# Optimization experiments

Measured on AMD Instinct MI355X. Metric: run time of the kernel, lower is better.

Reference implementation:

```python
import jax, jax.numpy as jnp
import numpy as np

N, E, D, H, SEQ = 50000, 600000, 128, 128, 50


def _gcn(x, W, b, src, dst):
    # PyG GCNConv: D^{-1/2}(A+I)D^{-1/2} X W + b, edge weights = 1
    n = x.shape[0]
    h = x @ W  # [N, H]
    deg = jnp.zeros((n,), x.dtype).at[dst].add(1.0) + 1.0  # +1 for self loop
    dinv = jax.lax.rsqrt(deg)
    norm = dinv[src] * dinv[dst]  # [E]
    agg = jnp.zeros_like(h).at[dst].add(h[src] * norm[:, None])
    agg = agg + h * (dinv * dinv)[:, None]  # self-loop contribution
    return agg + b


def _lstm_layer(xs, w_ih, w_hh, b_ih, b_hh):
    # xs: [B, T, I]; PyTorch gate order i, f, g, o
    B = xs.shape[0]
    Hh = w_hh.shape[1]
    bias = b_ih + b_hh

    def step(carry, x_t):
        h, c = carry
        g = x_t @ w_ih.T + h @ w_hh.T + bias
        i, f, gg, o = jnp.split(g, 4, axis=-1)
        c = jax.nn.sigmoid(f) * c + jax.nn.sigmoid(i) * jnp.tanh(gg)
        h = jax.nn.sigmoid(o) * jnp.tanh(c)
        return (h, c), h

    init = (jnp.zeros((B, Hh), xs.dtype), jnp.zeros((B, Hh), xs.dtype))
    _, hs = jax.lax.scan(step, init, xs.transpose(1, 0, 2))
    return hs.transpose(1, 0, 2)  # [B, T, H]


def setup_inputs() -> dict:
    key = jax.random.key(0)
    ks = jax.random.split(key, 16)
    s = 1.0 / np.sqrt(H)
    inp = {
        "x": jax.random.normal(ks[0], (N, D), jnp.float32),
        "edge_index": jax.random.randint(ks[1], (2, E), 0, N, jnp.int64),
        "sequence_length": SEQ,
        "W1": jax.random.normal(ks[2], (D, H), jnp.float32) * s,
        "b1": jnp.zeros((H,), jnp.float32),
        "W2": jax.random.normal(ks[3], (H, H), jnp.float32) * s,
        "b2": jnp.zeros((H,), jnp.float32),
        "fc_w": jax.random.normal(ks[4], (1, H), jnp.float32) * s,
        "fc_b": jnp.zeros((1,), jnp.float32),
    }
    for l in range(2):
        inp[f"w_ih{l}"] = jax.random.normal(ks[5 + 4 * l], (4 * H, H), jnp.float32) * s
        inp[f"w_hh{l}"] = jax.random.normal(ks[6 + 4 * l], (4 * H, H), jnp.float32) * s
        inp[f"b_ih{l}"] = jax.random.normal(ks[7 + 4 * l], (4 * H,), jnp.float32) * s
        inp[f"b_hh{l}"] = jax.random.normal(ks[8 + 4 * l], (4 * H,), jnp.float32) * s
    return inp


def reference(x, edge_index, sequence_length, W1, b1, W2, b2,
              w_ih0, w_hh0, b_ih0, b_hh0, w_ih1, w_hh1, b_ih1, b_hh1,
              fc_w, fc_b):
    src, dst = edge_index[0], edge_index[1]
    h = jax.nn.relu(_gcn(x, W1, b1, src, dst))   # dropout is identity in eval
    h = jax.nn.relu(_gcn(h, W2, b2, src, dst))
    seq = h.reshape(-1, sequence_length, h.shape[-1])  # [B, T, H]
    seq = _lstm_layer(seq, w_ih0, w_hh0, b_ih0, b_hh0)
    seq = _lstm_layer(seq, w_ih1, w_hh1, b_ih1, b_hh1)
    last = seq[:, -1, :]
    return last @ fc_w.T + fc_b  # [B, 1]
```

## Files before the change

### kernel.cpp

```cpp
#include <hip/hip_runtime.h>

#define NND 50000
#define NE  600000
#define TSEQ 50
#define NB  1000
#define SB  4
#define AHS 136
#define NSCB 196

typedef __attribute__((ext_vector_type(4))) float f32x4;
typedef __attribute__((ext_vector_type(8))) short s16x8;

__device__ __forceinline__ float sigf(float x) {
    return __builtin_amdgcn_rcpf(1.0f + __expf(-x));
}
__device__ __forceinline__ float tanhfast(float x) {
    x = fminf(fmaxf(x, -15.f), 15.f);
    float e = __expf(2.f * x);
    return (e - 1.f) * __builtin_amdgcn_rcpf(e + 1.f);
}
__device__ __forceinline__ unsigned short f2bf(float f) {
    unsigned int u = __float_as_uint(f);
    u = u + 0x7FFFu + ((u >> 16) & 1u);
    return (unsigned short)(u >> 16);
}
__device__ __forceinline__ float bf2f(unsigned short h) {
    return __uint_as_float(((unsigned int)h) << 16);
}
__device__ __forceinline__ void barrier_lds_only() {
    asm volatile("s_waitcnt lgkmcnt(0)\n\ts_barrier" ::: "memory");
}
__device__ __forceinline__ int grow_perm(int n) {
    int grp = n / 200;
    int rem = n % 200;
    return grp * 200 + (n % 50) * 4 + rem / 50;
}

__global__ void k_count(const int* __restrict__ ei, int* __restrict__ cnt) {
    int e = blockIdx.x * 256 + threadIdx.x;
    if (e < NE) atomicAdd(&cnt[ei[NE + e]], 1);
}

__global__ __launch_bounds__(256) void k_bsum(const int* __restrict__ cnt,
                                              int* __restrict__ bsum) {
    __shared__ int red[256];
    int t = threadIdx.x;
    int idx = blockIdx.x * 256 + t;
    red[t] = (idx < NND) ? cnt[idx] : 0;
    __syncthreads();
    for (int off = 128; off > 0; off >>= 1) {
        if (t < off) red[t] += red[t + off];
        __syncthreads();
    }
    if (t == 0) bsum[blockIdx.x] = red[0];
}

__global__ __launch_bounds__(256) void k_bscan(int* __restrict__ bsum) {
    __shared__ int ps[256];
    int t = threadIdx.x;
    int v = (t < NSCB) ? bsum[t] : 0;
    ps[t] = v;
    __syncthreads();
    for (int off = 1; off < 256; off <<= 1) {
        int u = 0;
        if (t >= off) u = ps[t - off];
        __syncthreads();
        if (t >= off) ps[t] += u;
        __syncthreads();
    }
    if (t < NSCB) bsum[t] = ps[t] - v;
}

__global__ __launch_bounds__(256) void k_bout(const int* __restrict__ cnt,
                                              const int* __restrict__ bsum,
                                              int* __restrict__ rowstart,
                                              float* __restrict__ dinv) {
    __shared__ int ps[256];
    int t = threadIdx.x;
    int idx = blockIdx.x * 256 + t;
    int v = (idx < NND) ? cnt[idx] : 0;
    ps[t] = v;
    __syncthreads();
    for (int off = 1; off < 256; off <<= 1) {
        int u = 0;
        if (t >= off) u = ps[t - off];
        __syncthreads();
        if (t >= off) ps[t] += u;
        __syncthreads();
    }
    int boff = bsum[blockIdx.x];
    if (idx < NND) {
        rowstart[idx] = boff + ps[t] - v;
        dinv[idx] = 1.0f / sqrtf((float)v + 1.0f);
    }
    if (idx == NND - 1) rowstart[NND] = boff + ps[t];
}

__global__ void k_fill(const int* __restrict__ ei, const int* __restrict__ rowstart,
                       int* __restrict__ cursor, int* __restrict__ adj) {
    int e = blockIdx.x * 256 + threadIdx.x;
    if (e >= NE) return;
    int s = ei[e], d = ei[NE + e];
    int pos = atomicAdd(&cursor[d], 1);
    adj[rowstart[d] + pos] = s;
}

__global__ __launch_bounds__(256) void k_gemm_mfma_h2(
    const unsigned short* __restrict__ Ahi,
    const unsigned short* __restrict__ Bhi, const unsigned short* __restrict__ Blo,
    const float* __restrict__ bias, unsigned short* __restrict__ C,
    int M, int Nc, int NT)
{
    __shared__ unsigned short As_hi[128][136];

    const int tid  = threadIdx.x;
    const int lane = tid & 63, wave = tid >> 6;
    const int mw = wave & 1, nw = wave >> 1;
    const int l15 = lane & 15, quad = lane >> 4;
    const int rowBase = blockIdx.y * 128;

    {
        int r0 = tid >> 4;
        int ko = (tid & 15) * 8;
        #pragma unroll
        for (int i = 0; i < 8; ++i) {
            int row = r0 + i * 16;
            int g = rowBase + row;
            uint4 vh = make_uint4(0, 0, 0, 0);
            if (g < M) vh = *(const uint4*)&Ahi[(size_t)g * 128 + ko];
            *(uint4*)&As_hi[row][ko] = vh;
        }
    }
    __syncthreads();

    for (int nt = 0; nt < NT; ++nt) {
        const int colBase = (blockIdx.x * NT + nt) * 64;

        s16x8 bh[2][4], bl[2][4];
        #pragma unroll
        for (int ns = 0; ns < 2; ++ns) {
            int gn = colBase + nw * 32 + ns * 16 + l15;
            #pragma unroll
            for (int kq = 0; kq < 4; ++kq) {
                bh[ns][kq] = *(const s16x8*)&Bhi[(size_t)gn * 128 + kq * 32 + quad * 8];
                bl[ns][kq] = *(const s16x8*)&Blo[(size_t)gn * 128 + kq * 32 + quad * 8];
            }
        }

        f32x4 acc[4][2] = {};
        #pragma unroll
        for (int kq = 0; kq < 4; ++kq) {
            int kof = kq * 32 + quad * 8;
            s16x8 ah[4];
            #pragma unroll
            for (int ms = 0; ms < 4; ++ms) {
                int r = mw * 64 + ms * 16 + l15;
                ah[ms] = *(const s16x8*)&As_hi[r][kof];
            }
            #pragma unroll
            for (int ms = 0; ms < 4; ++ms)
                #pragma unroll
                for (int ns = 0; ns < 2; ++ns)
                    acc[ms][ns] = __builtin_amdgcn_mfma_f32_16x16x32_bf16(ah[ms], bh[ns][kq], acc[ms][ns], 0, 0, 0);
            #pragma unroll
            for (int ms = 0; ms < 4; ++ms)
                #pragma unroll
                for (int ns = 0; ns < 2; ++ns)
                    acc[ms][ns] = __builtin_amdgcn_mfma_f32_16x16x32_bf16(ah[ms], bl[ns][kq], acc[ms][ns], 0, 0, 0);
        }

        #pragma unroll
        for (int ns = 0; ns < 2; ++ns) {
            int col = colBase + nw * 32 + ns * 16 + l15;
            float bv = bias ? bias[col] : 0.f;
            #pragma unroll
            for (int ms = 0; ms < 4; ++ms) {
                int row0 = rowBase + mw * 64 + ms * 16 + quad * 4;
                #pragma unroll
                for (int r = 0; r < 4; ++r) {
                    int row = row0 + r;
                    if (row < M) C[(size_t)row * Nc + col] = f2bf(acc[ms][ns][r] + bv);
                }
            }
        }
    }
}

__global__ __launch_bounds__(256) void k_gemm_mfma_xa(
    const float* __restrict__ X,
    const unsigned short* __restrict__ Bhi, const unsigned short* __restrict__ Blo,
    const float* __restrict__ bias, unsigned short* __restrict__ C,
    int M, int Nc, int NT)
{
    __shared__ unsigned short As_hi[128][136];
    __shared__ unsigned short As_lo[128][136];

    const int tid  = threadIdx.x;
    const int lane = tid & 63, wave = tid >> 6;
    const int mw = wave & 1, nw = wave >> 1;
    const int l15 = lane & 15, quad = lane >> 4;
    const int rowBase = blockIdx.y * 128;

    {
        int r0 = tid >> 4;
        int ko = (tid & 15) * 8;
        #pragma unroll
        for (int i = 0; i < 8; ++i) {
            int row = r0 + i * 16;
            int g = rowBase + row;
            unsigned short hx[8], lx[8];
            if (g < M) {
                float4 v0 = *(const float4*)&X[(size_t)g * 128 + ko];
                float4 v1 = *(const float4*)&X[(size_t)g * 128 + ko + 4];
                const float vv[8] = {v0.x, v0.y, v0.z, v0.w, v1.x, v1.y, v1.z, v1.w};
                #pragma unroll
                for (int e = 0; e < 8; ++e) {
                    hx[e] = f2bf(vv[e]);
                    lx[e] = f2bf(vv[e] - bf2f(hx[e]));
                }
            } else {
                #pragma unroll
                for (int e = 0; e < 8; ++e) { hx[e] = 0; lx[e] = 0; }
            }
            *(uint4*)&As_hi[row][ko] = *(const uint4*)hx;
            *(uint4*)&As_lo[row][ko] = *(const uint4*)lx;
        }
    }
    __syncthreads();

    for (int nt = 0; nt < NT; ++nt) {
        const int colBase = (blockIdx.x * NT + nt) * 64;

        s16x8 bh[2][4], bl[2][4];
        #pragma unroll
        for (int ns = 0; ns < 2; ++ns) {
            int gn = colBase + nw * 32 + ns * 16 + l15;
            #pragma unroll
            for (int kq = 0; kq < 4; ++kq) {
                bh[ns][kq] = *(const s16x8*)&Bhi[(size_t)gn * 128 + kq * 32 + quad * 8];
                bl[ns][kq] = *(const s16x8*)&Blo[(size_t)gn * 128 + kq * 32 + quad * 8];
            }
        }

        f32x4 acc[4][2] = {};
        #pragma unroll
        for (int kq = 0; kq < 4; ++kq) {
            int kof = kq * 32 + quad * 8;
            s16x8 ah[4], al[4];
            #pragma unroll
            for (int ms = 0; ms < 4; ++ms) {
                int r = mw * 64 + ms * 16 + l15;
                ah[ms] = *(const s16x8*)&As_hi[r][kof];
                al[ms] = *(const s16x8*)&As_lo[r][kof];
            }
            #pragma unroll
            for (int ms = 0; ms < 4; ++ms)
                #pragma unroll
                for (int ns = 0; ns < 2; ++ns)
                    acc[ms][ns] = __builtin_amdgcn_mfma_f32_16x16x32_bf16(ah[ms], bh[ns][kq], acc[ms][ns], 0, 0, 0);
            #pragma unroll
            for (int ms = 0; ms < 4; ++ms)
                #pragma unroll
                for (int ns = 0; ns < 2; ++ns)
                    acc[ms][ns] = __builtin_amdgcn_mfma_f32_16x16x32_bf16(al[ms], bh[ns][kq], acc[ms][ns], 0, 0, 0);
            #pragma unroll
            for (int ms = 0; ms < 4; ++ms)
                #pragma unroll
                for (int ns = 0; ns < 2; ++ns)
                    acc[ms][ns] = __builtin_amdgcn_mfma_f32_16x16x32_bf16(ah[ms], bl[ns][kq], acc[ms][ns], 0, 0, 0);
        }

        #pragma unroll
        for (int ns = 0; ns < 2; ++ns) {
            int col = colBase + nw * 32 + ns * 16 + l15;
            float bv = bias ? bias[col] : 0.f;
            #pragma unroll
            for (int ms = 0; ms < 4; ++ms) {
                int row0 = rowBase + mw * 64 + ms * 16 + quad * 4;
                #pragma unroll
                for (int r = 0; r < 4; ++r) {
                    int row = row0 + r;
                    if (row < M) C[(size_t)row * Nc + col] = f2bf(acc[ms][ns][r] + bv);
                }
            }
        }
    }
}

__global__ __launch_bounds__(512, 1) void k_gemm_gT_h(
    const unsigned short* __restrict__ Ahi,
    const unsigned short* __restrict__ Whi, const unsigned short* __restrict__ Wlo,
    const float* __restrict__ bp, unsigned short* __restrict__ G,
    int M)
{
    __shared__ unsigned short As_hi[64][136];

    const int tid  = threadIdx.x;
    const int lane = tid & 63, wave = tid >> 6;
    const int l15 = lane & 15, quad = lane >> 4;
    const int rowBase = blockIdx.x * 64;
    const int pb = wave * 64;

    s16x8 wh[2][2][4], wl[2][2][4];
    #pragma unroll
    for (int tp = 0; tp < 2; ++tp)
        #pragma unroll
        for (int t = 0; t < 2; ++t)
            #pragma unroll
            for (int kq = 0; kq < 4; ++kq) {
                const size_t wrow = (size_t)(pb + tp * 32 + t * 16 + l15) * 128 + kq * 32 + quad * 8;
                wh[tp][t][kq] = *(const s16x8*)&Whi[wrow];
                wl[tp][t][kq] = *(const s16x8*)&Wlo[wrow];
            }

    {
        int r0 = tid >> 3;
        int ko = (tid & 7) * 8;
        int g = rowBase + r0;
        uint4 v0 = make_uint4(0, 0, 0, 0), v1 = make_uint4(0, 0, 0, 0);
        if (g < M) {
            v0 = *(const uint4*)&Ahi[(size_t)g * 128 + ko];
            v1 = *(const uint4*)&Ahi[(size_t)g * 128 + ko + 64];
        }
        *(uint4*)&As_hi[r0][ko] = v0;
        *(uint4*)&As_hi[r0][ko + 64] = v1;
    }
    __syncthreads();

    float4 bv[2][2];
    #pragma unroll
    for (int tp = 0; tp < 2; ++tp)
        #pragma unroll
        for (int t = 0; t < 2; ++t)
            bv[tp][t] = *(const float4*)&bp[pb + tp * 32 + t * 16 + quad * 4];

    #pragma unroll
    for (int tp = 0; tp < 2; ++tp) {
        const int p0 = pb + tp * 32;
        #pragma unroll
        for (int rg = 0; rg < 4; ++rg) {
            s16x8 xh[4];
            #pragma unroll
            for (int kq = 0; kq < 4; ++kq)
                xh[kq] = *(const s16x8*)&As_hi[rg * 16 + l15][kq * 32 + quad * 8];
            f32x4 acc[2] = {};
            #pragma unroll
            for (int kq = 0; kq < 4; ++kq)
                #pragma unroll
                for (int t = 0; t < 2; ++t) {
                    acc[t] = __builtin_amdgcn_mfma_f32_16x16x32_bf16(wh[tp][t][kq], xh[kq], acc[t], 0, 0, 0);
                    acc[t] = __builtin_amdgcn_mfma_f32_16x16x32_bf16(wl[tp][t][kq], xh[kq], acc[t], 0, 0, 0);
                }
            const int row = rowBase + rg * 16 + l15;
            if (row < M) {
                const size_t prow = (size_t)grow_perm(row);
                #pragma unroll
                for (int t = 0; t < 2; ++t) {
                    ushort4 o;
                    o.x = f2bf(acc[t][0] + bv[tp][t].x);
                    o.y = f2bf(acc[t][1] + bv[tp][t].y);
                    o.z = f2bf(acc[t][2] + bv[tp][t].z);
                    o.w = f2bf(acc[t][3] + bv[tp][t].w);
                    *(ushort4*)&G[prow * 512 + p0 + t * 16 + quad * 4] = o;
                }
            }
        }
    }
}

__global__ __launch_bounds__(256) void k_gather(
    const int* __restrict__ rowstart, const int* __restrict__ adj,
    const unsigned short* __restrict__ h, const float* __restrict__ dinv,
    const float* __restrict__ bias,
    unsigned short* __restrict__ hi)
{
    const int n    = blockIdx.x * 4 + (threadIdx.x >> 6);
    const int lane = threadIdx.x & 63;
    const int r0 = rowstart[n], r1 = rowstart[n + 1];
    const float dn = dinv[n];

    ushort2 hv = *(const ushort2*)&h[(size_t)n * 128 + 2 * lane];
    float2 acc;
    acc.x = bf2f(hv.x) * dn;
    acc.y = bf2f(hv.y) * dn;

    int i = r0;
    for (; i + 4 <= r1; i += 4) {
        int s0 = adj[i], s1 = adj[i + 1], s2 = adj[i + 2], s3 = adj[i + 3];
        float d0 = dinv[s0], d1 = dinv[s1], d2 = dinv[s2], d3 = dinv[s3];
        ushort2 v0 = *(const ushort2*)&h[(size_t)s0 * 128 + 2 * lane];
        ushort2 v1 = *(const ushort2*)&h[(size_t)s1 * 128 + 2 * lane];
        ushort2 v2 = *(const ushort2*)&h[(size_t)s2 * 128 + 2 * lane];
        ushort2 v3 = *(const ushort2*)&h[(size_t)s3 * 128 + 2 * lane];
        acc.x += bf2f(v0.x) * d0; acc.y += bf2f(v0.y) * d0;
        acc.x += bf2f(v1.x) * d1; acc.y += bf2f(v1.y) * d1;
        acc.x += bf2f(v2.x) * d2; acc.y += bf2f(v2.y) * d2;
        acc.x += bf2f(v3.x) * d3; acc.y += bf2f(v3.y) * d3;
    }
    for (; i < r1; ++i) {
        int s = adj[i];
        float ds = dinv[s];
        ushort2 v = *(const ushort2*)&h[(size_t)s * 128 + 2 * lane];
        acc.x += bf2f(v.x) * ds;
        acc.y += bf2f(v.y) * ds;
    }

    float2 bb = *(const float2*)&bias[2 * lane];
    float vx = fmaxf(acc.x * dn + bb.x, 0.f);
    float vy = fmaxf(acc.y * dn + bb.y, 0.f);
    ushort2 ho;
    ho.x = f2bf(vx);
    ho.y = f2bf(vy);
    *(ushort2*)&hi[(size_t)n * 128 + 2 * lane] = ho;
}

__global__ void k_prep_gcnw2(const float* __restrict__ W1, const float* __restrict__ W2,
                             unsigned short* __restrict__ hi1, unsigned short* __restrict__ lo1,
                             unsigned short* __restrict__ hi2, unsigned short* __restrict__ lo2) {
    int t = blockIdx.x * 256 + threadIdx.x;
    const float* W = (t < 16384) ? W1 : W2;
    unsigned short* hi = (t < 16384) ? hi1 : hi2;
    unsigned short* lo = (t < 16384) ? lo1 : lo2;
    int tt = t & 16383;
    int k = tt >> 7, n = tt & 127;
    float v = W[tt];
    unsigned short h = f2bf(v);
    hi[n * 128 + k] = h;
    lo[n * 128 + k] = f2bf(v - bf2f(h));
}

__global__ void k_prep_lstm(const float* __restrict__ w_ih, const float* __restrict__ w_hh,
                            const float* __restrict__ b_ih, const float* __restrict__ b_hh,
                            unsigned short* __restrict__ ih_hi, unsigned short* __restrict__ ih_lo,
                            unsigned short* __restrict__ hh_hi, unsigned short* __restrict__ hh_lo,
                            float* __restrict__ bp)
{
    int t = blockIdx.x * 256 + threadIdx.x;
    if (t < 65536) {
        int r = t >> 7, k = t & 127;
        int g = r >> 7, j = r & 127;
        int p = (j << 2) + g;
        float v = w_ih[t];
        unsigned short h = f2bf(v);
        ih_hi[p * 128 + k] = h;
        ih_lo[p * 128 + k] = f2bf(v - bf2f(h));
    } else if (t < 131072) {
        int t2 = t - 65536;
        int r = t2 >> 7, k = t2 & 127;
        int g = r >> 7, j = r & 127;
        int p = (j << 2) + g;
        float v = w_hh[t2];
        unsigned short h = f2bf(v);
        hh_hi[p * 128 + k] = h;
        hh_lo[p * 128 + k] = f2bf(v - bf2f(h));
    } else if (t < 131584) {
        int r = t - 131072;
        int g = r >> 7, j = r & 127;
        bp[(j << 2) + g] = b_ih[r] + b_hh[r];
    }
}

__global__ __launch_bounds__(512, 2) void k_lstm(
    const unsigned short* __restrict__ G,
    const unsigned short* __restrict__ Whi,
    unsigned short* __restrict__ Hhi,
    const float* __restrict__ fcw,
    const float* __restrict__ fcb,
    float* __restrict__ outp)
{
    const int tid  = threadIdx.x;
    const int lane = tid & 63, wave = tid >> 6;
    const int l15  = lane & 15, quad = lane >> 4;
    const int b0   = blockIdx.x * SB;

    __shared__ __align__(16) unsigned short Ah[16 * AHS];
    __shared__ float partw[8][4][72];

    const int nt0 = wave * 4;
    s16x8 bh[4][4];
    #pragma unroll
    for (int nt = 0; nt < 4; ++nt) {
        int p = (nt0 + nt) * 16 + l15;
        #pragma unroll
        for (int ks = 0; ks < 4; ++ks)
            bh[nt][ks] = *(const s16x8*)&Whi[(size_t)p * 128 + ks * 32 + quad * 8];
    }

    for (int i = tid; i < 16 * AHS; i += 512) Ah[i] = 0;

    const int b2 = lane >> 4;
    const int jj = wave * 16 + l15;
    const int bg = b0 + b2;
    float c = 0.f;
    float hn_last = 0.f;

    const unsigned short* gb = &G[((size_t)blockIdx.x * 200 + b2) * 512 + (jj << 2)];
    ushort4 gr_cur = *(const ushort4*)&gb[0];
    unsigned short* hptr = Hhi ? &Hhi[(size_t)bg * TSEQ * 128 + jj] : nullptr;

    __syncthreads();

    for (int step = 0; step < TSEQ; ++step) {
        const int nstep = (step + 1 < TSEQ) ? step + 1 : step;
        const ushort4 gr_nxt = *(const ushort4*)&gb[(size_t)nstep * 2048];

        f32x4 acc[4] = {};
        #pragma unroll
        for (int ks = 0; ks < 4; ++ks) {
            s16x8 ah = *(const s16x8*)&Ah[l15 * AHS + ks * 32 + quad * 8];
            #pragma unroll
            for (int nt = 0; nt < 4; ++nt)
                acc[nt] = __builtin_amdgcn_mfma_f32_16x16x32_bf16(ah, bh[nt][ks], acc[nt], 0, 0, 0);
        }

        if (quad == 0) {
            #pragma unroll
            for (int nt = 0; nt < 4; ++nt)
                #pragma unroll
                for (int r = 0; r < 4; ++r)
                    partw[wave][r][nt * 16 + l15] = acc[nt][r];
        }

        {
            float4 pa = *(const float4*)&partw[wave][b2][l15 * 4];
            float xi = pa.x + bf2f(gr_cur.x);
            float xf = pa.y + bf2f(gr_cur.y);
            float xg = pa.z + bf2f(gr_cur.z);
            float xo = pa.w + bf2f(gr_cur.w);
            float ii = sigf(xi), ff = sigf(xf), gg = tanhfast(xg), oo = sigf(xo);
            float cn = ff * c + ii * gg;
            c = cn;
            float hn = oo * tanhfast(cn);
            hn_last = hn;
            unsigned short hh = f2bf(hn);
            Ah[b2 * AHS + jj] = hh;
            if (hptr) {
                *hptr = hh;
                hptr += 128;
            }
        }
        gr_cur = gr_nxt;
        barrier_lds_only();
    }

    if (outp) {
        float* red = (float*)Ah;
        red[b2 * 128 + jj] = hn_last * fcw[jj];
        __syncthreads();
        if (wave < 4) {
            float v = red[wave * 128 + lane] + red[wave * 128 + lane + 64];
            #pragma unroll
            for (int off = 32; off > 0; off >>= 1)
                v += __shfl_down(v, off);
            if (lane == 0) outp[b0 + wave] = v + fcb[0];
        }
    }
}

extern "C" void kernel_launch(void* const* d_in, const int* in_sizes, int n_in,
                              void* d_out, int out_size, void* d_ws, size_t ws_size,
                              hipStream_t stream)
{
    const float* x    = (const float*)d_in[0];
    const int*   ei   = (const int*)d_in[1];
    const float* W1   = (const float*)d_in[3];
    const float* b1   = (const float*)d_in[4];
    const float* W2   = (const float*)d_in[5];
    const float* b2   = (const float*)d_in[6];
    const float* fcw  = (const float*)d_in[7];
    const float* fcb  = (const float*)d_in[8];
    const float* wih0 = (const float*)d_in[9];
    const float* whh0 = (const float*)d_in[10];
    const float* bih0 = (const float*)d_in[11];
    const float* bhh0 = (const float*)d_in[12];
    const float* wih1 = (const float*)d_in[13];
    const float* whh1 = (const float*)d_in[14];
    const float* bih1 = (const float*)d_in[15];
    const float* bhh1 = (const float*)d_in[16];
    float* out = (float*)d_out;

    char* ws = (char*)d_ws;
    unsigned short* shi = (unsigned short*)(ws + 0);
    unsigned short* bufG = (unsigned short*)(ws + 51200000);

    unsigned short* xhi = (unsigned short*)(ws + 51200000);
    unsigned short* bufHg = (unsigned short*)(ws + 76800000);
    int* cnt      = (int*)(ws + 102400000);
    int* cursor   = (int*)(ws + 102604800);
    int* rowstart = (int*)(ws + 102809600);
    int* adj      = (int*)(ws + 103014400);
    int* bsum     = (int*)(ws + 105420800);

    float* dinv = (float*)(ws + 153600000);
    float* bp0  = (float*)(ws + 153800192);
    float* bp1  = (float*)(ws + 153802240);
    unsigned short* w1t_hi   = (unsigned short*)(ws + 153804288);
    unsigned short* w1t_lo   = (unsigned short*)(ws + 153837056);
    unsigned short* w2t_hi   = (unsigned short*)(ws + 153869824);
    unsigned short* w2t_lo   = (unsigned short*)(ws + 153902592);
    unsigned short* wpih0_hi = (unsigned short*)(ws + 153935360);
    unsigned short* wpih0_lo = (unsigned short*)(ws + 154066432);
    unsigned short* wpih1_hi = (unsigned short*)(ws + 154197504);
    unsigned short* wpih1_lo = (unsigned short*)(ws + 154328576);
    unsigned short* wphh0_hi = (unsigned short*)(ws + 154459648);
    unsigned short* wphh0_lo = (unsigned short*)(ws + 154590720);
    unsigned short* wphh1_hi = (unsigned short*)(ws + 154721792);
    unsigned short* wphh1_lo = (unsigned short*)(ws + 154852864);

    hipMemsetAsync(cnt, 0, 409600, stream);
    k_count<<<(NE + 255) / 256, 256, 0, stream>>>(ei, cnt);
    k_bsum<<<NSCB, 256, 0, stream>>>(cnt, bsum);
    k_bscan<<<1, 256, 0, stream>>>(bsum);
    k_bout<<<NSCB, 256, 0, stream>>>(cnt, bsum, rowstart, dinv);
    k_fill<<<(NE + 255) / 256, 256, 0, stream>>>(ei, rowstart, cursor, adj);

    k_prep_gcnw2<<<128, 256, 0, stream>>>(W1, W2, w1t_hi, w1t_lo, w2t_hi, w2t_lo);
    k_prep_lstm<<<514, 256, 0, stream>>>(wih0, whh0, bih0, bhh0,
                                         wpih0_hi, wpih0_lo, wphh0_hi, wphh0_lo, bp0);
    k_prep_lstm<<<514, 256, 0, stream>>>(wih1, whh1, bih1, bhh1,
                                         wpih1_hi, wpih1_lo, wphh1_hi, wphh1_lo, bp1);

    dim3 gH(1, 391);

    k_gemm_mfma_xa<<<gH, 256, 0, stream>>>(x, w1t_hi, w1t_lo, nullptr, bufHg, NND, 128, 2);
    k_gather<<<NND / 4, 256, 0, stream>>>(rowstart, adj, bufHg, dinv, b1, xhi);

    k_gemm_mfma_h2<<<gH, 256, 0, stream>>>(xhi, w2t_hi, w2t_lo, nullptr, bufHg, NND, 128, 2);
    k_gather<<<NND / 4, 256, 0, stream>>>(rowstart, adj, bufHg, dinv, b2, shi);

    k_gemm_gT_h<<<782, 512, 0, stream>>>(shi, wpih0_hi, wpih0_lo, bp0, bufG, NND);
    k_lstm<<<NB / SB, 512, 0, stream>>>(bufG, wphh0_hi, shi,
                                        nullptr, nullptr, nullptr);

    k_gemm_gT_h<<<782, 512, 0, stream>>>(shi, wpih1_hi, wpih1_lo, bp1, bufG, NND);
    k_lstm<<<NB / SB, 512, 0, stream>>>(bufG, wphh1_hi, nullptr,
                                        fcw, fcb, out);
}
```

Measured before the change: 460.3 us.

## Process four 64-row tiles per block in gate GEMM with double-buffered LDS

The input-to-gate GEMM now has each 512-thread block handle 256 rows instead of 64. Weights and bias stay loaded in registers across four tiles, and the next A tile is prefetched into a second LDS buffer while the current one is computed. The goal is to amortise the per-block weight register load (hi and lo splits) and overlap global loads with MFMA work. The grid shrinks to about 196 blocks, which may leave some of the GPU's compute units underused.

```diff
diff --git a/kernel.cpp b/kernel.cpp
--- a/kernel.cpp
+++ b/kernel.cpp
@@ -293,78 +293,84 @@
     const float* __restrict__ bp, unsigned short* __restrict__ G,
     int M)
 {
-    __shared__ unsigned short As_hi[64][136];
+    __shared__ unsigned short As[2][64][136];
 
     const int tid  = threadIdx.x;
     const int lane = tid & 63, wave = tid >> 6;
     const int l15 = lane & 15, quad = lane >> 4;
-    const int rowBase = blockIdx.x * 64;
+    const int rowBase0 = blockIdx.x * 256;
     const int pb = wave * 64;
 
-    s16x8 wh[2][2][4], wl[2][2][4];
+    s16x8 wh[4][4], wl[4][4];
     #pragma unroll
-    for (int tp = 0; tp < 2; ++tp)
-        #pragma unroll
-        for (int t = 0; t < 2; ++t)
-            #pragma unroll
-            for (int kq = 0; kq < 4; ++kq) {
-                const size_t wrow = (size_t)(pb + tp * 32 + t * 16 + l15) * 128 + kq * 32 + quad * 8;
-                wh[tp][t][kq] = *(const s16x8*)&Whi[wrow];
-                wl[tp][t][kq] = *(const s16x8*)&Wlo[wrow];
-            }
+    for (int t = 0; t < 4; ++t)
+        #pragma unroll
+        for (int kq = 0; kq < 4; ++kq) {
+            const size_t wrow = (size_t)(pb + t * 16 + l15) * 128 + kq * 32 + quad * 8;
+            wh[t][kq] = *(const s16x8*)&Whi[wrow];
+            wl[t][kq] = *(const s16x8*)&Wlo[wrow];
+        }
+    float4 bv[4];
+    #pragma unroll
+    for (int t = 0; t < 4; ++t)
+        bv[t] = *(const float4*)&bp[pb + t * 16 + quad * 4];
 
     {
-        int r0 = tid >> 3;
-        int ko = (tid & 7) * 8;
-        int g = rowBase + r0;
+        int r0 = tid >> 3, ko = (tid & 7) * 8;
+        int g = rowBase0 + r0;
         uint4 v0 = make_uint4(0, 0, 0, 0), v1 = make_uint4(0, 0, 0, 0);
         if (g < M) {
             v0 = *(const uint4*)&Ahi[(size_t)g * 128 + ko];
             v1 = *(const uint4*)&Ahi[(size_t)g * 128 + ko + 64];
         }
-        *(uint4*)&As_hi[r0][ko] = v0;
-        *(uint4*)&As_hi[r0][ko + 64] = v1;
+        *(uint4*)&As[0][r0][ko] = v0;
+        *(uint4*)&As[0][r0][ko + 64] = v1;
     }
     __syncthreads();
 
-    float4 bv[2][2];
     #pragma unroll
-    for (int tp = 0; tp < 2; ++tp)
-        #pragma unroll
-        for (int t = 0; t < 2; ++t)
-            bv[tp][t] = *(const float4*)&bp[pb + tp * 32 + t * 16 + quad * 4];
-
-    #pragma unroll
-    for (int tp = 0; tp < 2; ++tp) {
-        const int p0 = pb + tp * 32;
+    for (int p = 0; p < 4; ++p) {
+        const int cur = p & 1;
+        if (p < 3) {
+            int r0 = tid >> 3, ko = (tid & 7) * 8;
+            int g = rowBase0 + (p + 1) * 64 + r0;
+            uint4 v0 = make_uint4(0, 0, 0, 0), v1 = make_uint4(0, 0, 0, 0);
+            if (g < M) {
+                v0 = *(const uint4*)&Ahi[(size_t)g * 128 + ko];
+                v1 = *(const uint4*)&Ahi[(size_t)g * 128 + ko + 64];
+            }
+            *(uint4*)&As[cur ^ 1][r0][ko] = v0;
+            *(uint4*)&As[cur ^ 1][r0][ko + 64] = v1;
+        }
+
+        const int rowBase = rowBase0 + p * 64;
         #pragma unroll
         for (int rg = 0; rg < 4; ++rg) {
             s16x8 xh[4];
             #pragma unroll
             for (int kq = 0; kq < 4; ++kq)
-                xh[kq] = *(const s16x8*)&As_hi[rg * 16 + l15][kq * 32 + quad * 8];
-            f32x4 acc[2] = {};
-            #pragma unroll
-            for (int kq = 0; kq < 4; ++kq)
-                #pragma unroll
-                for (int t = 0; t < 2; ++t) {
-                    acc[t] = __builtin_amdgcn_mfma_f32_16x16x32_bf16(wh[tp][t][kq], xh[kq], acc[t], 0, 0, 0);
-                    acc[t] = __builtin_amdgcn_mfma_f32_16x16x32_bf16(wl[tp][t][kq], xh[kq], acc[t], 0, 0, 0);
+                xh[kq] = *(const s16x8*)&As[cur][rg * 16 + l15][kq * 32 + quad * 8];
+            const int row = rowBase + rg * 16 + l15;
+            const size_t prow = (row < M) ? (size_t)grow_perm(row) : 0;
+            #pragma unroll
+            for (int t = 0; t < 4; ++t) {
+                f32x4 acc = {};
+                #pragma unroll
+                for (int kq = 0; kq < 4; ++kq) {
+                    acc = __builtin_amdgcn_mfma_f32_16x16x32_bf16(wh[t][kq], xh[kq], acc, 0, 0, 0);
+                    acc = __builtin_amdgcn_mfma_f32_16x16x32_bf16(wl[t][kq], xh[kq], acc, 0, 0, 0);
                 }
-            const int row = rowBase + rg * 16 + l15;
-            if (row < M) {
-                const size_t prow = (size_t)grow_perm(row);
-                #pragma unroll
-                for (int t = 0; t < 2; ++t) {
+                if (row < M) {
                     ushort4 o;
-                    o.x = f2bf(acc[t][0] + bv[tp][t].x);
-                    o.y = f2bf(acc[t][1] + bv[tp][t].y);
-                    o.z = f2bf(acc[t][2] + bv[tp][t].z);
-                    o.w = f2bf(acc[t][3] + bv[tp][t].w);
-                    *(ushort4*)&G[prow * 512 + p0 + t * 16 + quad * 4] = o;
+                    o.x = f2bf(acc[0] + bv[t].x);
+                    o.y = f2bf(acc[1] + bv[t].y);
+                    o.z = f2bf(acc[2] + bv[t].z);
+                    o.w = f2bf(acc[3] + bv[t].w);
+                    *(ushort4*)&G[prow * 512 + pb + t * 16 + quad * 4] = o;
                 }
             }
         }
+        __syncthreads();
     }
 }
 
@@ -621,6 +627,7 @@
                                          wpih1_hi, wpih1_lo, wphh1_hi, wphh1_lo, bp1);
 
     dim3 gH(1, 391);
+    const int gGate = (NND + 255) / 256;
 
     k_gemm_mfma_xa<<<gH, 256, 0, stream>>>(x, w1t_hi, w1t_lo, nullptr, bufHg, NND, 128, 2);
     k_gather<<<NND / 4, 256, 0, stream>>>(rowstart, adj, bufHg, dinv, b1, xhi);
@@ -628,11 +635,11 @@
     k_gemm_mfma_h2<<<gH, 256, 0, stream>>>(xhi, w2t_hi, w2t_lo, nullptr, bufHg, NND, 128, 2);
     k_gather<<<NND / 4, 256, 0, stream>>>(rowstart, adj, bufHg, dinv, b2, shi);
 
-    k_gemm_gT_h<<<782, 512, 0, stream>>>(shi, wpih0_hi, wpih0_lo, bp0, bufG, NND);
+    k_gemm_gT_h<<<gGate, 512, 0, stream>>>(shi, wpih0_hi, wpih0_lo, bp0, bufG, NND);
     k_lstm<<<NB / SB, 512, 0, stream>>>(bufG, wphh0_hi, shi,
                                         nullptr, nullptr, nullptr);
 
-    k_gemm_gT_h<<<782, 512, 0, stream>>>(shi, wpih1_hi, wpih1_lo, bp1, bufG, NND);
+    k_gemm_gT_h<<<gGate, 512, 0, stream>>>(shi, wpih1_hi, wpih1_lo, bp1, bufG, NND);
     k_lstm<<<NB / SB, 512, 0, stream>>>(bufG, wphh1_hi, nullptr,
                                         fcw, fcb, out);
 }
```

After: 417.4 us (median of 2 runs). 1.1x faster.
